# Kernel tuning notes

Measured on AMD Instinct MI355X. Metric: run time of the kernel, lower is better.

The kernel has to match this reference:

```python
import jax, jax.numpy as jnp
from jax import lax
import numpy as np
import math

B, LBL, PRED, CIN = 16, 48, 336, 7
L = LBL + PRED
DM, E = 512, 2
DIN, N, DCONV = 2 * DM, 16, 4
DTR = math.ceil(DM / 16)  # 32
TF = 4  # freq='h' time features
EPS = 1e-5


def _ln(x, w, b):
    m = x.mean(-1, keepdims=True)
    v = ((x - m) ** 2).mean(-1, keepdims=True)
    return (x - m) / jnp.sqrt(v + EPS) * w + b


def _silu(x):
    return x * jax.nn.sigmoid(x)


def _token_embed(x, w):
    # Conv1d(c_in, d_model, k=3, padding=1, circular, bias=False). x: (B,L,C), w: (DM,C,3)
    xp = jnp.concatenate([x[:, -1:], x, x[:, :1]], axis=1)  # circular pad along L
    y = lax.conv_general_dilated(xp.transpose(0, 2, 1), w, (1,), 'VALID',
                                 dimension_numbers=('NCH', 'OIH', 'NCH'))
    return y.transpose(0, 2, 1)  # (B,L,DM)


def _selective_scan(u, dt, A, Bm, Cm):
    # u,dt: (B,L,DIN); A: (DIN,N); Bm,Cm: (B,L,N)
    h0 = jnp.zeros((u.shape[0], DIN, N), u.dtype)

    def step(h, inp):
        u_t, dt_t, B_t, C_t = inp  # (B,DIN),(B,DIN),(B,N),(B,N)
        dA = jnp.exp(dt_t[:, :, None] * A)  # (B,DIN,N)
        h = dA * h + (dt_t * u_t)[:, :, None] * B_t[:, None, :]
        y = jnp.einsum('bdn,bn->bd', h, C_t)
        return h, y

    _, ys = lax.scan(step, h0, (u.transpose(1, 0, 2), dt.transpose(1, 0, 2),
                                Bm.transpose(1, 0, 2), Cm.transpose(1, 0, 2)))
    return ys.transpose(1, 0, 2)  # (B,L,DIN)


def _mamba(x, p):
    (in_w, conv_w, conv_b, xproj_w, dtproj_w, dtproj_b, A_log, Dp, out_w) = p
    xz = x @ in_w.T                      # (B,L,2*DIN)
    xin, z = jnp.split(xz, 2, axis=-1)
    # depthwise causal conv1d, kernel DCONV
    xt = jnp.pad(xin.transpose(0, 2, 1), ((0, 0), (0, 0), (DCONV - 1, 0)))
    xc = lax.conv_general_dilated(xt, conv_w, (1,), 'VALID', feature_group_count=DIN,
                                  dimension_numbers=('NCH', 'OIH', 'NCH'))
    xc = _silu((xc + conv_b[None, :, None]).transpose(0, 2, 1))  # (B,L,DIN)
    dbc = xc @ xproj_w.T                 # (B,L,DTR+2N)
    dt_r, Bm, Cm = dbc[..., :DTR], dbc[..., DTR:DTR + N], dbc[..., DTR + N:]
    dt = jax.nn.softplus(dt_r @ dtproj_w.T + dtproj_b)  # (B,L,DIN)
    A = -jnp.exp(A_log)                  # (DIN,N)
    y = _selective_scan(xc, dt, A, Bm, Cm) + xc * Dp
    y = y * _silu(z)
    return y @ out_w.T                   # (B,L,DM)


def _model(x_dec, x_mark_dec, token_w, timef_w, layer_ps, fin_w, fin_b, out_w):
    mean = lax.stop_gradient(x_dec[:, :LBL].mean(1, keepdims=True))
    head = x_dec[:, :LBL] - mean
    std = lax.stop_gradient(jnp.sqrt(head.var(axis=1, keepdims=True) + EPS))
    head = head / std
    xd = jnp.concatenate([head, x_dec[:, LBL:]], axis=1)
    x = _token_embed(xd, token_w) + x_mark_dec @ timef_w.T  # DataEmbedding_wo_pos (eval: no dropout)
    for i in range(E):
        nw, nb = layer_ps[0][i], layer_ps[1][i]
        mp = tuple(layer_ps[j][i] for j in range(2, 11))
        x = x + _mamba(_ln(x, nw, nb), mp)
    x = _ln(x, fin_w, fin_b)
    out = x @ out_w.T
    out = out * std + mean
    return out[:, -PRED:, :]


def setup_inputs() -> dict:
    key = jax.random.key(0)
    ks = jax.random.split(key, 20)
    s = 0.02
    d = {
        'x_enc': jax.random.normal(ks[0], (B, 96, CIN), jnp.float32),
        'x_mark_enc': jax.random.normal(ks[1], (B, 96, TF), jnp.float32),
        'x_dec': jax.random.normal(ks[2], (B, L, CIN), jnp.float32),
        'x_mark_dec': jax.random.normal(ks[3], (B, L, TF), jnp.float32),
        'token_w': jax.random.normal(ks[4], (DM, CIN, 3), jnp.float32) * s,
        'timef_w': jax.random.normal(ks[5], (DM, TF), jnp.float32) * s,
        'norm_w': jnp.ones((E, DM), jnp.float32),
        'norm_b': jnp.zeros((E, DM), jnp.float32),
        'in_proj_w': jax.random.normal(ks[6], (E, 2 * DIN, DM), jnp.float32) * s,
        'conv_w': jax.random.normal(ks[7], (E, DIN, 1, DCONV), jnp.float32) * s,
        'conv_b': jnp.zeros((E, DIN), jnp.float32),
        'xproj_w': jax.random.normal(ks[8], (E, DTR + 2 * N, DIN), jnp.float32) * s,
        'dtproj_w': jax.random.normal(ks[9], (E, DIN, DTR), jnp.float32) * s,
        'dtproj_b': jnp.full((E, DIN), -4.0, jnp.float32),
        'A_log': jnp.tile(jnp.log(jnp.arange(1, N + 1, dtype=jnp.float32)), (E, DIN, 1)),
        'D': jnp.ones((E, DIN), jnp.float32),
        'outproj_w': jax.random.normal(ks[10], (E, DM, DIN), jnp.float32) * s,
        'final_norm_w': jnp.ones((DM,), jnp.float32),
        'final_norm_b': jnp.zeros((DM,), jnp.float32),
        'out_w': jax.random.normal(ks[11], (CIN, DM), jnp.float32) * s,
    }
    return d


def reference(x_enc, x_mark_enc, x_dec, x_mark_dec, token_w, timef_w, norm_w, norm_b,
              in_proj_w, conv_w, conv_b, xproj_w, dtproj_w, dtproj_b, A_log, D,
              outproj_w, final_norm_w, final_norm_b, out_w):
    layer_ps = (norm_w, norm_b, in_proj_w, conv_w, conv_b, xproj_w, dtproj_w,
                dtproj_b, A_log, D, outproj_w)
    return _model(x_dec, x_mark_dec, token_w, timef_w, layer_ps,
                  final_norm_w, final_norm_b, out_w)
```

## Files before the change

### kernel.cpp

```cpp
#include <hip/hip_runtime.h>

#define B_    16
#define LBL_  48
#define PRED_ 336
#define CIN_  7
#define L_    384
#define DM_   512
#define E_    2
#define DIN_  1024
#define N_    16
#define DCONV_ 4
#define DTR_  32
#define TF_   4
#define EPSF  1e-5f
#define NSEG  16
#define SEGL  24
#define SC2   2
#define NCHK  12

typedef unsigned short u16;
typedef __attribute__((ext_vector_type(8))) short short8;
typedef __attribute__((ext_vector_type(4))) float f32x4;

__device__ __forceinline__ float bf2f(u16 u){
  union { float f; unsigned int i; } cv; cv.i = ((unsigned int)u) << 16; return cv.f;
}
__device__ __forceinline__ u16 f2bf(float f){
  union { float f; unsigned int i; } cv; cv.f = f;
  unsigned int x = cv.i;
  unsigned int lsb = (x >> 16) & 1u;
  x += 0x7fffu + lsb;
  return (u16)(x >> 16);
}
__device__ __forceinline__ float lo16(unsigned int v){
  union { float f; unsigned int i; } cv; cv.i = v << 16; return cv.f;
}
__device__ __forceinline__ float hi16(unsigned int v){
  union { float f; unsigned int i; } cv; cv.i = v & 0xffff0000u; return cv.f;
}

#define GLDS(g, l) __builtin_amdgcn_global_load_lds( \
    (const __attribute__((address_space(1))) void*)(g), \
    (__attribute__((address_space(3))) void*)(l), 16, 0, 0)

#define PO_XDEC   0
#define PO_XMARK  43008
#define PO_TOKW   67584
#define PO_TIMEF  78336
#define PO_NORMW  80384
#define PO_NORMB  81408
#define PO_INW    82432
#define PO_CONVW  2179584
#define PO_CONVB  2187776
#define PO_XPROJ  2189824
#define PO_DTW    2320896
#define PO_DTB    2386432
#define PO_ALOG   2388480
#define PO_DP     2421248
#define PO_OUTW   2423296
#define PO_FNW    3471872
#define PO_FNB    3472384
#define PO_HEADW  3472896
#define P_TOTAL   3476480
#define A_X    3476480
#define A_LNB  6622208
#define A_XZ   9767936
#define A_DT   22350848
#define A_DBCS 28642304
#define A_MEAN 29078528
#define A_STD  29078640
#define A_XCB_OFF 3145728

struct Ptrs { const void* p[18]; };

__device__ __forceinline__ float wredsum(float s){
  #pragma unroll
  for (int off = 32; off; off >>= 1) s += __shfl_xor(s, off, 64);
  return s;
}

__device__ __forceinline__ void qpowers(float q, float* p){
  float q2 = q*q;
  float q4 = q2*q2;
  float q8 = q4*q4;
  float q3 = q2*q;
  p[0]=q;      p[1]=q2;     p[2]=q3;     p[3]=q4;
  p[4]=q4*q;   p[5]=q4*q2;  p[6]=q4*q3;  p[7]=q8;
  p[8]=q8*q;   p[9]=q8*q2;  p[10]=q8*q3; p[11]=q8*q4;
  p[12]=q8*p[4]; p[13]=q8*p[5]; p[14]=q8*p[6]; p[15]=q8*q8;
}

__device__ __forceinline__ unsigned int xcd_swz(unsigned int bid, unsigned int nwg){
  return (bid & 7u) * (nwg >> 3) + (bid >> 3);
}

__global__ __launch_bounds__(256) void convert_kernel(Ptrs ps, float* __restrict__ dst){
  const int offs[18] = {PO_XDEC, PO_XMARK, PO_TOKW, PO_TIMEF, PO_NORMW, PO_NORMB,
                        PO_INW, PO_CONVW, PO_CONVB, PO_XPROJ, PO_DTW, PO_DTB,
                        PO_ALOG, PO_DP, PO_OUTW, PO_FNW, PO_FNB, PO_HEADW};
  int idx = blockIdx.x * 256 + threadIdx.x;
  if (idx >= P_TOTAL) return;
  int seg = 0;
  #pragma unroll
  for (int s = 1; s < 18; s++) if (idx >= offs[s]) seg = s;
  int off = idx - offs[seg];
  int isbf = (((const u16*)ps.p[4])[0] == 0x3F80u);
  if (seg == 6 || seg == 9 || seg == 10 || seg == 14){
    u16 hv = isbf ? ((const u16*)ps.p[seg])[off]
                  : f2bf(((const float*)ps.p[seg])[off]);
    ((u16*)(dst + offs[seg]))[off] = hv;
  } else {
    float v = isbf ? bf2f(((const u16*)ps.p[seg])[off])
                   : ((const float*)ps.p[seg])[off];
    dst[idx] = v;
  }
}

__global__ __launch_bounds__(256) void embed_ln_kernel(const float* __restrict__ x_dec,
      const float* __restrict__ token_w, const float* __restrict__ x_mark,
      const float* __restrict__ timef_w, const float* __restrict__ nw,
      const float* __restrict__ nb, float* __restrict__ x, u16* __restrict__ out,
      float* __restrict__ meanv, float* __restrict__ stdv){
  __shared__ float sm[8], siv[8], ssd[8];
  int wv = threadIdx.x >> 6;
  int lane = threadIdx.x & 63;
  int tok = blockIdx.x*4 + wv;
  int t = tok % L_;
  int b = tok / L_;
  for (int c = wv; c < CIN_; c += 4){
    float v0 = (lane < LBL_) ? x_dec[(b*L_+lane)*CIN_+c] : 0.f;
    float m = wredsum(v0) * (1.f/LBL_);
    float dv = (lane < LBL_) ? (v0 - m) : 0.f;
    float sd = sqrtf(wredsum(dv*dv) * (1.f/LBL_) + EPSF);
    if (lane == 0){ sm[c] = m; siv[c] = 1.f/sd; ssd[c] = sd; }
  }
  __syncthreads();
  if ((blockIdx.x % (L_/4)) == 0 && threadIdx.x < CIN_){
    meanv[b*CIN_ + threadIdx.x] = sm[threadIdx.x];
    stdv[b*CIN_ + threadIdx.x]  = ssd[threadIdx.x];
  }
  int tm1 = (t == 0) ? L_-1 : t-1;
  int tp1 = (t == L_-1) ? 0 : t+1;
  auto ldx = [&](int row, int c){
    float v = x_dec[(b*L_+row)*CIN_+c];
    return (row < LBL_) ? (v - sm[c]) * siv[c] : v;
  };
  const float* mk = x_mark + (b*L_+t)*TF_;
  float a0[CIN_], a1[CIN_], a2[CIN_], mkv[TF_];
  #pragma unroll
  for (int ci = 0; ci < CIN_; ci++){ a0[ci]=ldx(tm1,ci); a1[ci]=ldx(t,ci); a2[ci]=ldx(tp1,ci); }
  #pragma unroll
  for (int f = 0; f < TF_; f++) mkv[f] = mk[f];
  float v[8];
  #pragma unroll
  for (int j = 0; j < 8; j++){
    int d = lane*8 + j;
    float acc = 0.f;
    #pragma unroll
    for (int ci = 0; ci < CIN_; ci++){
      const float* w = token_w + (d*CIN_+ci)*3;
      acc += a0[ci]*w[0] + a1[ci]*w[1] + a2[ci]*w[2];
    }
    #pragma unroll
    for (int f = 0; f < TF_; f++)
      acc += mkv[f] * timef_w[d*TF_+f];
    v[j] = acc;
  }
  float* xr = x + (size_t)tok*DM_ + lane*8;
  *(float4*)xr       = (float4){v[0],v[1],v[2],v[3]};
  *(float4*)(xr + 4) = (float4){v[4],v[5],v[6],v[7]};
  float s = (v[0]+v[1])+(v[2]+v[3])+((v[4]+v[5])+(v[6]+v[7]));
  float mean = wredsum(s) * (1.f/DM_);
  float s2 = 0.f;
  #pragma unroll
  for (int j = 0; j < 8; j++){ v[j] -= mean; s2 += v[j]*v[j]; }
  float rstd = rsqrtf(wredsum(s2) * (1.f/DM_) + EPSF);
  const float* wr = nw + lane*8;
  const float* br = nb + lane*8;
  uint4 o; unsigned int* op = (unsigned int*)&o;
  #pragma unroll
  for (int k = 0; k < 4; k++){
    u16 e0 = f2bf(v[2*k]   * rstd * wr[2*k]   + br[2*k]);
    u16 e1 = f2bf(v[2*k+1] * rstd * wr[2*k+1] + br[2*k+1]);
    op[k] = (unsigned int)e0 | ((unsigned int)e1 << 16);
  }
  *(uint4*)(out + (size_t)tok*DM_ + lane*8) = o;
}

__global__ __launch_bounds__(256) void ln_kernel(const float* __restrict__ x,
     const float* __restrict__ w, const float* __restrict__ bias, u16* __restrict__ out){
  int tok = blockIdx.x*4 + (threadIdx.x >> 6);
  int lane = threadIdx.x & 63;
  const float* xr = x + (size_t)tok*DM_ + lane*8;
  float4 a = *(const float4*)xr;
  float4 bq = *(const float4*)(xr + 4);
  float v[8] = {a.x,a.y,a.z,a.w,bq.x,bq.y,bq.z,bq.w};
  float s = (v[0]+v[1])+(v[2]+v[3])+((v[4]+v[5])+(v[6]+v[7]));
  float mean = wredsum(s) * (1.f/DM_);
  float s2 = 0.f;
  #pragma unroll
  for (int j = 0; j < 8; j++){ v[j] -= mean; s2 += v[j]*v[j]; }
  float rstd = rsqrtf(wredsum(s2) * (1.f/DM_) + EPSF);
  const float* wr = w + lane*8;
  const float* br = bias + lane*8;
  uint4 o; unsigned int* op = (unsigned int*)&o;
  #pragma unroll
  for (int k = 0; k < 4; k++){
    u16 e0 = f2bf(v[2*k]   * rstd * wr[2*k]   + br[2*k]);
    u16 e1 = f2bf(v[2*k+1] * rstd * wr[2*k+1] + br[2*k+1]);
    op[k] = (unsigned int)e0 | ((unsigned int)e1 << 16);
  }
  *(uint4*)(out + (size_t)tok*DM_ + lane*8) = o;
}

__global__ __launch_bounds__(256) void inproj_conv(const u16* __restrict__ A,
    const u16* __restrict__ Wt, const float* __restrict__ cw, const float* __restrict__ cb,
    u16* __restrict__ xz, u16* __restrict__ xcb){
  __shared__ u16 As[384 * 64];
  __shared__ u16 Ws[64 * 64];
  int tid = threadIdx.x;
  int wv = tid >> 6, lane = tid & 63;
  unsigned int bid = blockIdx.y * 32 + blockIdx.x;
  unsigned int swz = xcd_swz(bid, 512);
  int b  = (int)(swz >> 5);
  int n0 = (int)(swz & 31) * 64;
  int m0 = b * L_;
  int la = lane & 15, lk = lane >> 4;
  f32x4 acc[6][4];
  #pragma unroll
  for (int i = 0; i < 6; i++)
    #pragma unroll
    for (int j = 0; j < 4; j++) acc[i][j] = (f32x4){0.f,0.f,0.f,0.f};
  int sr = lane >> 3;
  int sc = (((lane & 7) ^ (sr & 7)) * 8);
  const u16* Ag = A + (size_t)(m0 + wv*96 + sr) * DM_ + sc;
  u16* Al = As + (wv*96)*64 + lane*8;
  const u16* Wg = Wt + (size_t)(n0 + wv*16 + sr) * DM_ + sc;
  u16* Wl = Ws + (wv*16)*64 + lane*8;
  for (int k0 = 0; k0 < DM_; k0 += 64){
    #pragma unroll
    for (int i = 0; i < 12; i++) GLDS(Ag + (size_t)(i*8)*DM_ + k0, Al + i*512);
    #pragma unroll
    for (int i = 0; i < 2; i++)  GLDS(Wg + (size_t)(i*8)*DM_ + k0, Wl + i*512);
    __syncthreads();
    #pragma unroll
    for (int ks = 0; ks < 2; ks++){
      int ch = (ks*4 + lk) ^ (la & 7);
      short8 af[6], bfr[4];
      #pragma unroll
      for (int mi = 0; mi < 6; mi++) af[mi] = *(const short8*)&As[(wv*96 + mi*16 + la)*64 + ch*8];
      #pragma unroll
      for (int ni = 0; ni < 4; ni++) bfr[ni] = *(const short8*)&Ws[(ni*16 + la)*64 + ch*8];
      #pragma unroll
      for (int mi = 0; mi < 6; mi++)
        #pragma unroll
        for (int ni = 0; ni < 4; ni++)
          acc[mi][ni] = __builtin_amdgcn_mfma_f32_16x16x32_bf16(af[mi], bfr[ni], acc[mi][ni], 0, 0, 0);
    }
    __syncthreads();
  }
  #pragma unroll
  for (int mi = 0; mi < 6; mi++)
    #pragma unroll
    for (int ni = 0; ni < 4; ni++){
      int colc = ni*2 + (la >> 3);
      #pragma unroll
      for (int r = 0; r < 4; r++){
        int row = wv*96 + mi*16 + lk*4 + r;
        As[row*64 + ((colc ^ (row & 7))<<3) + (la & 7)] = f2bf(acc[mi][ni][r]);
      }
    }
  __syncthreads();
  int c8 = (tid & 7) * 8;
  int tg = tid >> 3;
  if (n0 < DIN_){
    float4 w[8]; float bias[8];
    #pragma unroll
    for (int k = 0; k < 8; k++){
      w[k] = *(const float4*)(cw + (n0 + c8 + k)*4);
      bias[k] = cb[n0 + c8 + k];
    }
    for (int i = 0; i < 12; i++){
      int t = tg*12 + i;
      uint4 tap[4];
      #pragma unroll
      for (int j = 0; j < 4; j++){
        int rr = t - 3 + j;
        if (rr >= 0)
          tap[j] = *(const uint4*)&As[rr*64 + ((((c8>>3) ^ (rr & 7)))<<3)];
      }
      float v[8];
      #pragma unroll
      for (int k = 0; k < 8; k++){
        float s = bias[k];
        #pragma unroll
        for (int j = 0; j < 4; j++){
          if (j >= 3 - t){
            const unsigned int* tp = (const unsigned int*)&tap[j];
            float xv = (k & 1) ? hi16(tp[k >> 1]) : lo16(tp[k >> 1]);
            s += xv * ((const float*)&w[k])[j];
          }
        }
        v[k] = s / (1.f + __expf(-s));
      }
      uint4 o; unsigned int* op = (unsigned int*)&o;
      #pragma unroll
      for (int k = 0; k < 4; k++)
        op[k] = (unsigned int)f2bf(v[2*k]) | ((unsigned int)f2bf(v[2*k+1]) << 16);
      *(uint4*)(xcb + (size_t)(m0 + t)*DIN_ + n0 + c8) = o;
    }
  } else {
    for (int i = 0; i < 12; i++){
      int t = tg*12 + i;
      uint4 vq = *(const uint4*)&As[t*64 + ((((c8>>3) ^ (t & 7)))<<3)];
      *(uint4*)(xz + (size_t)(m0 + t)*(2*DIN_) + n0 + c8) = vq;
    }
  }
}

template<int TN, int ACCUM, int BF16OUT>
__global__ __launch_bounds__(256) void gemm_mfma(const u16* __restrict__ A, const u16* __restrict__ Wt,
    void* __restrict__ C, int M, int N, int K){
  constexpr int WN = TN / 2;
  constexpr int NI = WN / 16;
  __shared__ u16 As[128 * 64];
  __shared__ u16 Ws[TN * 64];
  int tid = threadIdx.x;
  int wv = tid >> 6, lane = tid & 63;
  int wm = (wv & 1) * 64, wn = (wv >> 1) * WN;
  unsigned int gx = gridDim.x;
  unsigned int bid = blockIdx.y * gx + blockIdx.x;
  unsigned int swz = xcd_swz(bid, gx * gridDim.y);
  int m0 = (int)(swz / gx) * 128, n0 = (int)(swz % gx) * TN;
  int la = lane & 15, lk = lane >> 4;
  f32x4 acc[4][NI];
  #pragma unroll
  for (int i = 0; i < 4; i++)
    #pragma unroll
    for (int j = 0; j < NI; j++) acc[i][j] = (f32x4){0.f, 0.f, 0.f, 0.f};
  int sr = lane >> 3;
  int sc = (((lane & 7) ^ (sr & 7)) * 8);
  const u16* Ag = A + (size_t)(m0 + wv*32 + sr) * K + sc;
  u16* Al = As + (wv*32)*64 + lane*8;
  const u16 *Wg; u16 *Wl;
  if constexpr (TN == 128){
    Wg = Wt + (size_t)(n0 + wv*32 + sr) * K + sc;
    Wl = Ws + (wv*32)*64 + lane*8;
  } else {
    Wg = Wt + (size_t)(n0 + wv*16 + sr) * K + sc;
    Wl = Ws + (wv*16)*64 + lane*8;
  }
  for (int k0 = 0; k0 < K; k0 += 64){
    #pragma unroll
    for (int i = 0; i < 4; i++) GLDS(Ag + (size_t)(i*8)*K + k0, Al + i*512);
    if constexpr (TN == 128){
      #pragma unroll
      for (int i = 0; i < 4; i++) GLDS(Wg + (size_t)(i*8)*K + k0, Wl + i*512);
    } else {
      #pragma unroll
      for (int i = 0; i < 2; i++) GLDS(Wg + (size_t)(i*8)*K + k0, Wl + i*512);
    }
    __syncthreads();
    #pragma unroll
    for (int ks = 0; ks < 2; ks++){
      short8 af[4], bfr[NI];
      int ch = (ks*4 + lk) ^ (la & 7);
      #pragma unroll
      for (int mi = 0; mi < 4; mi++) af[mi] = *(const short8*)&As[(wm + mi*16 + la)*64 + ch*8];
      #pragma unroll
      for (int ni = 0; ni < NI; ni++) bfr[ni] = *(const short8*)&Ws[(wn + ni*16 + la)*64 + ch*8];
      #pragma unroll
      for (int mi = 0; mi < 4; mi++)
        #pragma unroll
        for (int ni = 0; ni < NI; ni++)
          acc[mi][ni] = __builtin_amdgcn_mfma_f32_16x16x32_bf16(af[mi], bfr[ni], acc[mi][ni], 0, 0, 0);
    }
    __syncthreads();
  }
  #pragma unroll
  for (int mi = 0; mi < 4; mi++)
    #pragma unroll
    for (int ni = 0; ni < NI; ni++){
      int row = m0 + wm + mi*16 + lk*4;
      int col = n0 + wn + ni*16 + la;
      #pragma unroll
      for (int r = 0; r < 4; r++){
        if constexpr (BF16OUT){
          u16* p = (u16*)C + (size_t)row * N + col;
          p[(size_t)r * N] = f2bf(acc[mi][ni][r]);
        } else {
          float* p = (float*)C + (size_t)row * N + col;
          if (ACCUM) p[(size_t)r * N] += acc[mi][ni][r];
          else       p[(size_t)r * N]  = acc[mi][ni][r];
        }
      }
    }
}

__global__ __launch_bounds__(256) void xdt_mfma(const u16* __restrict__ A,
    const u16* __restrict__ Wt, const u16* __restrict__ dtwb, const float* __restrict__ dtb,
    u16* __restrict__ dt, float* __restrict__ dbcs){
  __shared__ u16 As[32 * 64];
  __shared__ u16 Ws[64 * 64];
  __shared__ float Ds[32 * 66];
  __shared__ u16 Wd[64 * 32];
  __shared__ u16 Db[32 * 72];
  int tid = threadIdx.x;
  int wv = tid >> 6, lane = tid & 63;
  unsigned int swz = xcd_swz(blockIdx.x, 192);
  int m0 = (int)swz * 32;
  int la = lane & 15, lk = lane >> 4;
  int wm = (wv & 1) * 16, wn = (wv >> 1) * 32;

  f32x4 acc[2];
  acc[0] = (f32x4){0.f,0.f,0.f,0.f};
  acc[1] = (f32x4){0.f,0.f,0.f,0.f};
  int sr = lane >> 3;
  int sc = (((lane & 7) ^ (sr & 7)) * 8);
  const u16* Ag = A + (size_t)(m0 + wv*8 + sr) * DIN_ + sc;
  u16* Al = As + (wv*8)*64 + lane*8;
  const u16* Wg0 = Wt + (size_t)(wv*16 + sr) * DIN_ + sc;
  const u16* Wg1 = Wt + (size_t)(wv*16 + 8 + sr) * DIN_ + sc;
  u16* Wl0 = Ws + (wv*16)*64 + lane*8;
  u16* Wl1 = Ws + (wv*16 + 8)*64 + lane*8;
  for (int k0 = 0; k0 < DIN_; k0 += 64){
    GLDS(Ag + k0, Al);
    GLDS(Wg0 + k0, Wl0);
    GLDS(Wg1 + k0, Wl1);
    __syncthreads();
    #pragma unroll
    for (int ks = 0; ks < 2; ks++){
      int ch = (ks*4 + lk) ^ (la & 7);
      short8 af = *(const short8*)&As[(wm + la)*64 + ch*8];
      #pragma unroll
      for (int ni = 0; ni < 2; ni++){
        short8 bfr = *(const short8*)&Ws[(wn + ni*16 + la)*64 + ch*8];
        acc[ni] = __builtin_amdgcn_mfma_f32_16x16x32_bf16(af, bfr, acc[ni], 0, 0, 0);
      }
    }
    __syncthreads();
  }
  #pragma unroll
  for (int ni = 0; ni < 2; ni++)
    #pragma unroll
    for (int r = 0; r < 4; r++)
      Ds[(wm + lk*4 + r)*66 + wn + ni*16 + la] = acc[ni][r];
  __syncthreads();
  {
    int row = tid >> 3;
    int c4  = (tid & 7) * 4;
    float4 v = {Ds[row*66 + 32 + c4], Ds[row*66 + 33 + c4],
                Ds[row*66 + 34 + c4], Ds[row*66 + 35 + c4]};
    *(float4*)&dbcs[(size_t)(m0 + row)*32 + c4] = v;
  }
  short8 af2;
  {
    u16 tmp[8];
    #pragma unroll
    for (int i = 0; i < 8; i++)
      tmp[i] = f2bf(Ds[(wm + la)*66 + lk*8 + i]);
    af2 = *(const short8*)tmp;
  }

  int srd = lane >> 2;
  int scd = (((lane & 3) ^ (srd & 3)) * 8);
  for (int nt = 0; nt < 16; nt++){
    GLDS(dtwb + (size_t)(nt*64 + wv*16 + srd)*32 + scd, Wd + (wv*16)*32 + lane*8);
    __syncthreads();
    #pragma unroll
    for (int ni = 0; ni < 2; ni++){
      int rw = wn + ni*16 + la;
      int ch2 = (lk ^ (la & 3)) * 8;
      short8 bfr2 = *(const short8*)&Wd[rw*32 + ch2];
      f32x4 a2 = (f32x4){0.f,0.f,0.f,0.f};
      a2 = __builtin_amdgcn_mfma_f32_16x16x32_bf16(af2, bfr2, a2, 0, 0, 0);
      int d = nt*64 + wn + ni*16 + la;
      float bias = dtb[d];
      #pragma unroll
      for (int r = 0; r < 4; r++){
        float raw = a2[r] + bias;
        float sp = (raw > 20.f) ? raw : __logf(1.f + __expf(raw));
        Db[(wm + lk*4 + r)*72 + wn + ni*16 + la] = f2bf(sp);
      }
    }
    __syncthreads();
    int row = tid >> 3;
    int c8  = (tid & 7) * 8;
    uint4 o = *(const uint4*)&Db[row*72 + c8];
    *(uint4*)&dt[(size_t)(m0 + row)*DIN_ + nt*64 + c8] = o;
  }
}

#define WSTR2 896
__global__ __launch_bounds__(1024, 1) void scan_kernel(
    u16* __restrict__ ub_yb,
    const float* __restrict__ dbcs, const u16* __restrict__ xz,
    const u16* __restrict__ dtp,
    const float* __restrict__ A_log, const float* __restrict__ Dp){
  __shared__ float smem[16384];

  int tid = threadIdx.x;
  int lane = tid & 63;
  int seg  = tid >> 6;
  int b = blockIdx.x >> 4;
  int g = blockIdx.x & 15;
  int d = g*64 + lane;
  size_t base = (size_t)b * L_;

  float* wbase = smem + seg * WSTR2;
  float* sbc = wbase;
  float* su  = wbase + 128;
  float* sz  = wbase + 384;
  float* sdt = wbase + 640;

  int st = lane >> 5;
  int j  = lane & 31;

  float A[16];
  #pragma unroll
  for (int n = 0; n < 16; n += 4){
    float4 av = *(const float4*)(A_log + (size_t)d*N_ + n);
    A[n] = -__expf(av.x); A[n+1] = -__expf(av.y); A[n+2] = -__expf(av.z); A[n+3] = -__expf(av.w);
  }
  float Dv = Dp[d];
  bool fastA = true;
  #pragma unroll
  for (int n = 0; n < 16; n++) fastA = fastA && (fabsf(A[n] + (float)(n+1)) < 1e-3f*(n+1));

  float h[16];
  #pragma unroll
  for (int n = 0; n < 16; n++) h[n] = 0.f;

  auto ldc = [&](int c, float& kbc, unsigned int& ku, unsigned int& kz,
                 unsigned int& kt, bool wz){
    size_t tokr = base + seg*SEGL + c*SC2 + st;
    kbc = dbcs[tokr*32 + j];
    ku  = ((const unsigned int*)(ub_yb + tokr*DIN_ + g*64))[j];
    kt  = ((const unsigned int*)(dtp + tokr*DIN_ + g*64))[j];
    if (wz) kz = ((const unsigned int*)(xz + tokr*(2*DIN_) + DIN_ + g*64))[j];
  };
  auto stc = [&](int buf, float kbc, unsigned int ku, unsigned int kz,
                 unsigned int kt, bool wz){
    sbc[buf*64 + st*32 + j] = kbc;
    su [buf*128 + st*64 + 2*j]     = lo16(ku);
    su [buf*128 + st*64 + 2*j + 1] = hi16(ku);
    sdt[buf*128 + st*64 + 2*j]     = lo16(kt);
    sdt[buf*128 + st*64 + 2*j + 1] = hi16(kt);
    if (wz){
      sz[buf*128 + st*64 + 2*j]     = lo16(kz);
      sz[buf*128 + st*64 + 2*j + 1] = hi16(kz);
    }
  };

  float S = 0.f;
  {
    float kbc; unsigned int ku, kz, kt;
    ldc(0, kbc, ku, kz, kt, false);
    stc(0, kbc, ku, kz, kt, false);
    for (int c = 0; c < NCHK; c++){
      int cur = c & 1;
      bool have = (c + 1 < NCHK);
      float nbc; unsigned int nu, nz, nt;
      if (have) ldc(c+1, nbc, nu, nz, nt, false);
      for (int s = 0; s < SC2; s++){
        float dtv = sdt[cur*128 + s*64 + lane];
        float u   = su [cur*128 + s*64 + lane];
        const float* bcrow = sbc + cur*64 + s*32;
        float Bf[16];
        #pragma unroll
        for (int i = 0; i < 16; i += 4){
          float4 bv = *(const float4*)(bcrow + i);
          Bf[i] = bv.x; Bf[i+1] = bv.y; Bf[i+2] = bv.z; Bf[i+3] = bv.w;
        }
        float du = dtv * u;
        S += dtv;
        if (fastA){
          float q = __expf(-dtv);
          float p[16];
          qpowers(q, p);
          #pragma unroll
          for (int n = 0; n < 16; n++) h[n] = p[n] * h[n] + du * Bf[n];
        } else {
          #pragma unroll
          for (int n = 0; n < 16; n++){
            float dA = __expf(dtv * A[n]);
            h[n] = dA * h[n] + du * Bf[n];
          }
        }
      }
      if (have) stc(1 - cur, nbc, nu, nz, nt, false);
    }
  }

  #pragma unroll
  for (int half = 0; half < 2; half++){
    __syncthreads();
    #pragma unroll
    for (int n = 0; n < 8; n++){
      int nn = half*8 + n;
      smem[(n*NSEG + seg)*64 + lane]        = h[nn];
      smem[8192 + (n*NSEG + seg)*64 + lane] = __expf(A[nn] * S);
    }
    __syncthreads();
    float hs[8];
    #pragma unroll
    for (int n = 0; n < 8; n++) hs[n] = 0.f;
    for (int jj = 0; jj < seg; jj++){
      #pragma unroll
      for (int n = 0; n < 8; n++){
        float qh = smem[(n*NSEG + jj)*64 + lane];
        float qP = smem[8192 + (n*NSEG + jj)*64 + lane];
        hs[n] = qh + qP * hs[n];
      }
    }
    #pragma unroll
    for (int n = 0; n < 8; n++) h[half*8 + n] = hs[n];
  }
  __syncthreads();

  {
    float kbc; unsigned int ku, kz, kt;
    ldc(0, kbc, ku, kz, kt, true);
    stc(0, kbc, ku, kz, kt, true);
    for (int c = 0; c < NCHK; c++){
      int cur = c & 1;
      bool have = (c + 1 < NCHK);
      float nbc; unsigned int nu, nz, nt;
      if (have) ldc(c+1, nbc, nu, nz, nt, true);
      for (int s = 0; s < SC2; s++){
        float dtv = sdt[cur*128 + s*64 + lane];
        float u   = su [cur*128 + s*64 + lane];
        float z   = sz [cur*128 + s*64 + lane];
        const float* bcrow = sbc + cur*64 + s*32;
        float Bf[16], Cf[16];
        #pragma unroll
        for (int i = 0; i < 16; i += 4){
          float4 bv = *(const float4*)(bcrow + i);
          float4 cv = *(const float4*)(bcrow + 16 + i);
          Bf[i] = bv.x; Bf[i+1] = bv.y; Bf[i+2] = bv.z; Bf[i+3] = bv.w;
          Cf[i] = cv.x; Cf[i+1] = cv.y; Cf[i+2] = cv.z; Cf[i+3] = cv.w;
        }
        float du = dtv * u;
        float acc = 0.f;
        if (fastA){
          float q = __expf(-dtv);
          float p[16];
          qpowers(q, p);
          #pragma unroll
          for (int n = 0; n < 16; n++){
            h[n] = p[n] * h[n] + du * Bf[n];
            acc += h[n] * Cf[n];
          }
        } else {
          #pragma unroll
          for (int n = 0; n < 16; n++){
            float dA = __expf(dtv * A[n]);
            h[n] = dA * h[n] + du * Bf[n];
            acc += h[n] * Cf[n];
          }
        }
        float y = acc + u * Dv;
        size_t tok = base + seg*SEGL + c*SC2 + s;
        ub_yb[tok*DIN_ + d] = f2bf(y * (z / (1.f + __expf(-z))));
      }
      if (have) stc(1 - cur, nbc, nu, nz, nt, true);
    }
  }
}

__global__ __launch_bounds__(256) void head_kernel(const float* __restrict__ x,
    const float* __restrict__ fw, const float* __restrict__ fb, const float* __restrict__ ow,
    const float* __restrict__ meanv, const float* __restrict__ stdv, void* __restrict__ out,
    const u16* __restrict__ dtype_probe){
  int wav = blockIdx.x*4 + (threadIdx.x >> 6);
  int lane = threadIdx.x & 63;
  if (wav >= B_*PRED_) return;
  int b = wav / PRED_;
  int tt = wav % PRED_;
  int tok = b*L_ + LBL_ + tt;
  const float* xr = x + (size_t)tok*DM_ + lane*8;
  float4 a = *(const float4*)xr;
  float4 bq = *(const float4*)(xr + 4);
  float v[8] = {a.x,a.y,a.z,a.w,bq.x,bq.y,bq.z,bq.w};
  float s = (v[0]+v[1])+(v[2]+v[3])+((v[4]+v[5])+(v[6]+v[7]));
  float mean = wredsum(s) * (1.f/DM_);
  float s2 = 0.f;
  #pragma unroll
  for (int j = 0; j < 8; j++){ v[j] -= mean; s2 += v[j]*v[j]; }
  float rstd = rsqrtf(wredsum(s2) * (1.f/DM_) + EPSF);
  const float* fwr = fw + lane*8;
  const float* fbr = fb + lane*8;
  #pragma unroll
  for (int j = 0; j < 8; j++) v[j] = v[j] * rstd * fwr[j] + fbr[j];
  int isbf = (dtype_probe[0] == 0x3F80u);
  for (int o = 0; o < CIN_; o++){
    const float* owr = ow + (size_t)o*DM_ + lane*8;
    float part = 0.f;
    #pragma unroll
    for (int j = 0; j < 8; j++) part += v[j] * owr[j];
    part = wredsum(part);
    if (lane == 0){
      float res = part * stdv[b*CIN_ + o] + meanv[b*CIN_ + o];
      size_t oidx = (size_t)(b*PRED_ + tt)*CIN_ + o;
      if (isbf) ((u16*)out)[oidx] = f2bf(res);
      else      ((float*)out)[oidx] = res;
    }
  }
}

extern "C" void kernel_launch(void* const* d_in, const int* in_sizes, int n_in,
                              void* d_out, int out_size, void* d_ws, size_t ws_size,
                              hipStream_t stream){
  float* P = (float*)d_ws;

  Ptrs ps;
  for (int i = 0; i < 18; i++) ps.p[i] = d_in[2 + i];

  float* x    = P + A_X;
  u16*   lnxb = (u16*)(P + A_LNB);
  u16*   xz   = (u16*)(P + A_XZ);
  u16*   dt   = (u16*)(P + A_DT);
  u16*   xcb  = (u16*)(P + A_DT + A_XCB_OFF);
  float* dbcs = P + A_DBCS;
  float* meanv= P + A_MEAN;
  float* stdv = P + A_STD;
  const u16* bwi = (const u16*)(P + PO_INW);
  const u16* bwx = (const u16*)(P + PO_XPROJ);
  const u16* bwd = (const u16*)(P + PO_DTW);
  const u16* bwo = (const u16*)(P + PO_OUTW);

  convert_kernel<<<(P_TOTAL+255)/256, 256, 0, stream>>>(ps, P);
  embed_ln_kernel<<<(B_*L_)/4, 256, 0, stream>>>(
      P + PO_XDEC, P + PO_TOKW, P + PO_XMARK, P + PO_TIMEF,
      P + PO_NORMW, P + PO_NORMB, x, lnxb, meanv, stdv);

  for (int e = 0; e < E_; e++){
    if (e > 0)
      ln_kernel<<<(B_*L_)/4, 256, 0, stream>>>(x, P + PO_NORMW + e*DM_, P + PO_NORMB + e*DM_, lnxb);
    inproj_conv<<<dim3(32, 16), 256, 0, stream>>>(
        lnxb, bwi + (size_t)e*2*DIN_*DM_,
        P + PO_CONVW + e*DIN_*DCONV_, P + PO_CONVB + e*DIN_, xz, xcb);
    xdt_mfma<<<192, 256, 0, stream>>>(
        xcb, bwx + (size_t)e*64*DIN_, bwd + (size_t)e*DIN_*DTR_,
        P + PO_DTB + e*DIN_, dt, dbcs);
    scan_kernel<<<256, 1024, 0, stream>>>(
        xcb, dbcs, xz, dt, P + PO_ALOG + e*DIN_*N_, P + PO_DP + e*DIN_);
    gemm_mfma<64,1,0><<<dim3(DM_/64, (B_*L_)/128), 256, 0, stream>>>(
        xcb, bwo + (size_t)e*DM_*DIN_, x, B_*L_, DM_, DIN_);
  }

  head_kernel<<<(B_*PRED_+3)/4, 256, 0, stream>>>(
      x, P + PO_FNW, P + PO_FNB, P + PO_HEADW, meanv, stdv, d_out, (const u16*)d_in[6]);
}
```

Before: 379.5 us.

## Fuse parameter conversion into embedding kernel, vectorize conversion, reuse conv taps

Merges the weight-conversion kernel and the embedding/LayerNorm kernel into one launch. Embedding blocks read raw inputs directly in either dtype, and the remaining blocks convert parameters 8 elements per thread with vector loads and stores. The depthwise conv now slides a register window of taps instead of reloading four rows from LDS for each timestep. The head kernel batches its seven warp reductions into one interleaved shuffle loop. The cost is extra dtype branching inside the embedding path, and the conversion code now assumes every segment is aligned to 8 elements.

```diff
diff --git a/kernel.cpp b/kernel.cpp
--- a/kernel.cpp
+++ b/kernel.cpp
@@ -71,12 +71,21 @@
 #define A_STD  29078640
 #define A_XCB_OFF 3145728
 
+#define EMB_NB  ((B_*L_)/4)
+#define CV_BASE PO_NORMW
+#define CV_ELEMS (P_TOTAL - CV_BASE)
+#define CV_NB   ((CV_ELEMS + 2047)/2048)
+
 struct Ptrs { const void* p[18]; };
 
 __device__ __forceinline__ float wredsum(float s){
   #pragma unroll
   for (int off = 32; off; off >>= 1) s += __shfl_xor(s, off, 64);
   return s;
+}
+
+__device__ __forceinline__ float ldraw(const void* p, int i, int isbf){
+  return isbf ? bf2f(((const u16*)p)[i]) : ((const float*)p)[i];
 }
 
 __device__ __forceinline__ void qpowers(float q, float* p){
@@ -94,33 +103,58 @@
   return (bid & 7u) * (nwg >> 3) + (bid >> 3);
 }
 
-__global__ __launch_bounds__(256) void convert_kernel(Ptrs ps, float* __restrict__ dst){
-  const int offs[18] = {PO_XDEC, PO_XMARK, PO_TOKW, PO_TIMEF, PO_NORMW, PO_NORMB,
-                        PO_INW, PO_CONVW, PO_CONVB, PO_XPROJ, PO_DTW, PO_DTB,
-                        PO_ALOG, PO_DP, PO_OUTW, PO_FNW, PO_FNB, PO_HEADW};
-  int idx = blockIdx.x * 256 + threadIdx.x;
-  if (idx >= P_TOTAL) return;
-  int seg = 0;
-  #pragma unroll
-  for (int s = 1; s < 18; s++) if (idx >= offs[s]) seg = s;
-  int off = idx - offs[seg];
+__global__ __launch_bounds__(256) void prep_embed_convert(Ptrs ps, float* __restrict__ dst,
+      float* __restrict__ x, u16* __restrict__ out,
+      float* __restrict__ meanv, float* __restrict__ stdv){
   int isbf = (((const u16*)ps.p[4])[0] == 0x3F80u);
-  if (seg == 6 || seg == 9 || seg == 10 || seg == 14){
-    u16 hv = isbf ? ((const u16*)ps.p[seg])[off]
-                  : f2bf(((const float*)ps.p[seg])[off]);
-    ((u16*)(dst + offs[seg]))[off] = hv;
-  } else {
-    float v = isbf ? bf2f(((const u16*)ps.p[seg])[off])
-                   : ((const float*)ps.p[seg])[off];
-    dst[idx] = v;
-  }
-}
-
-__global__ __launch_bounds__(256) void embed_ln_kernel(const float* __restrict__ x_dec,
-      const float* __restrict__ token_w, const float* __restrict__ x_mark,
-      const float* __restrict__ timef_w, const float* __restrict__ nw,
-      const float* __restrict__ nb, float* __restrict__ x, u16* __restrict__ out,
-      float* __restrict__ meanv, float* __restrict__ stdv){
+  if ((int)blockIdx.x >= EMB_NB){
+    int idx0 = CV_BASE + ((int)blockIdx.x - EMB_NB)*2048 + (int)threadIdx.x*8;
+    if (idx0 >= P_TOTAL) return;
+    const int offs[14] = {PO_NORMW, PO_NORMB, PO_INW, PO_CONVW, PO_CONVB, PO_XPROJ,
+                          PO_DTW, PO_DTB, PO_ALOG, PO_DP, PO_OUTW, PO_FNW, PO_FNB, PO_HEADW};
+    const int wseg[14] = {0,0,1,0,0,1,1,0,0,0,1,0,0,0};
+    int seg = 0;
+    #pragma unroll
+    for (int s = 1; s < 14; s++) if (idx0 >= offs[s]) seg = s;
+    int off = idx0 - offs[seg];
+    const void* src = ps.p[seg + 4];
+    if (wseg[seg]){
+      if (isbf){
+        uint4 v = *(const uint4*)((const u16*)src + off);
+        *(uint4*)((u16*)(dst + offs[seg]) + off) = v;
+      } else {
+        float4 f0 = *(const float4*)((const float*)src + off);
+        float4 f1 = *(const float4*)((const float*)src + off + 4);
+        uint4 o; unsigned int* op = (unsigned int*)&o;
+        op[0] = (unsigned int)f2bf(f0.x) | ((unsigned int)f2bf(f0.y) << 16);
+        op[1] = (unsigned int)f2bf(f0.z) | ((unsigned int)f2bf(f0.w) << 16);
+        op[2] = (unsigned int)f2bf(f1.x) | ((unsigned int)f2bf(f1.y) << 16);
+        op[3] = (unsigned int)f2bf(f1.z) | ((unsigned int)f2bf(f1.w) << 16);
+        *(uint4*)((u16*)(dst + offs[seg]) + off) = o;
+      }
+    } else {
+      if (isbf){
+        uint4 v = *(const uint4*)((const u16*)src + off);
+        const u16* pv = (const u16*)&v;
+        float4 o0 = {bf2f(pv[0]), bf2f(pv[1]), bf2f(pv[2]), bf2f(pv[3])};
+        float4 o1 = {bf2f(pv[4]), bf2f(pv[5]), bf2f(pv[6]), bf2f(pv[7])};
+        *(float4*)(dst + idx0)     = o0;
+        *(float4*)(dst + idx0 + 4) = o1;
+      } else {
+        float4 f0 = *(const float4*)((const float*)src + off);
+        float4 f1 = *(const float4*)((const float*)src + off + 4);
+        *(float4*)(dst + idx0)     = f0;
+        *(float4*)(dst + idx0 + 4) = f1;
+      }
+    }
+    return;
+  }
+  const void* x_dec  = ps.p[0];
+  const void* x_mark = ps.p[1];
+  const void* tokw   = ps.p[2];
+  const void* timef  = ps.p[3];
+  const void* nw     = ps.p[4];
+  const void* nb     = ps.p[5];
   __shared__ float sm[8], siv[8], ssd[8];
   int wv = threadIdx.x >> 6;
   int lane = threadIdx.x & 63;
@@ -128,7 +162,7 @@
   int t = tok % L_;
   int b = tok / L_;
   for (int c = wv; c < CIN_; c += 4){
-    float v0 = (lane < LBL_) ? x_dec[(b*L_+lane)*CIN_+c] : 0.f;
+    float v0 = (lane < LBL_) ? ldraw(x_dec, (b*L_+lane)*CIN_+c, isbf) : 0.f;
     float m = wredsum(v0) * (1.f/LBL_);
     float dv = (lane < LBL_) ? (v0 - m) : 0.f;
     float sd = sqrtf(wredsum(dv*dv) * (1.f/LBL_) + EPSF);
@@ -142,15 +176,14 @@
   int tm1 = (t == 0) ? L_-1 : t-1;
   int tp1 = (t == L_-1) ? 0 : t+1;
   auto ldx = [&](int row, int c){
-    float v = x_dec[(b*L_+row)*CIN_+c];
+    float v = ldraw(x_dec, (b*L_+row)*CIN_+c, isbf);
     return (row < LBL_) ? (v - sm[c]) * siv[c] : v;
   };
-  const float* mk = x_mark + (b*L_+t)*TF_;
   float a0[CIN_], a1[CIN_], a2[CIN_], mkv[TF_];
   #pragma unroll
   for (int ci = 0; ci < CIN_; ci++){ a0[ci]=ldx(tm1,ci); a1[ci]=ldx(t,ci); a2[ci]=ldx(tp1,ci); }
   #pragma unroll
-  for (int f = 0; f < TF_; f++) mkv[f] = mk[f];
+  for (int f = 0; f < TF_; f++) mkv[f] = ldraw(x_mark, (b*L_+t)*TF_+f, isbf);
   float v[8];
   #pragma unroll
   for (int j = 0; j < 8; j++){
@@ -158,12 +191,13 @@
     float acc = 0.f;
     #pragma unroll
     for (int ci = 0; ci < CIN_; ci++){
-      const float* w = token_w + (d*CIN_+ci)*3;
-      acc += a0[ci]*w[0] + a1[ci]*w[1] + a2[ci]*w[2];
+      int wb = (d*CIN_+ci)*3;
+      acc += a0[ci]*ldraw(tokw, wb, isbf) + a1[ci]*ldraw(tokw, wb+1, isbf)
+           + a2[ci]*ldraw(tokw, wb+2, isbf);
     }
     #pragma unroll
     for (int f = 0; f < TF_; f++)
-      acc += mkv[f] * timef_w[d*TF_+f];
+      acc += mkv[f] * ldraw(timef, d*TF_+f, isbf);
     v[j] = acc;
   }
   float* xr = x + (size_t)tok*DM_ + lane*8;
@@ -175,13 +209,12 @@
   #pragma unroll
   for (int j = 0; j < 8; j++){ v[j] -= mean; s2 += v[j]*v[j]; }
   float rstd = rsqrtf(wredsum(s2) * (1.f/DM_) + EPSF);
-  const float* wr = nw + lane*8;
-  const float* br = nb + lane*8;
   uint4 o; unsigned int* op = (unsigned int*)&o;
   #pragma unroll
   for (int k = 0; k < 4; k++){
-    u16 e0 = f2bf(v[2*k]   * rstd * wr[2*k]   + br[2*k]);
-    u16 e1 = f2bf(v[2*k+1] * rstd * wr[2*k+1] + br[2*k+1]);
+    int d0 = lane*8 + 2*k;
+    u16 e0 = f2bf(v[2*k]   * rstd * ldraw(nw, d0,   isbf) + ldraw(nb, d0,   isbf));
+    u16 e1 = f2bf(v[2*k+1] * rstd * ldraw(nw, d0+1, isbf) + ldraw(nb, d0+1, isbf));
     op[k] = (unsigned int)e0 | ((unsigned int)e1 << 16);
   }
   *(uint4*)(out + (size_t)tok*DM_ + lane*8) = o;
@@ -280,14 +313,21 @@
       w[k] = *(const float4*)(cw + (n0 + c8 + k)*4);
       bias[k] = cb[n0 + c8 + k];
     }
+    uint4 tap[4];
+    {
+      int t0 = tg*12;
+      #pragma unroll
+      for (int j = 0; j < 4; j++){
+        int rr = t0 - 3 + j;
+        if (rr >= 0)
+          tap[j] = *(const uint4*)&As[rr*64 + ((((c8>>3) ^ (rr & 7)))<<3)];
+      }
+    }
     for (int i = 0; i < 12; i++){
       int t = tg*12 + i;
-      uint4 tap[4];
-      #pragma unroll
-      for (int j = 0; j < 4; j++){
-        int rr = t - 3 + j;
-        if (rr >= 0)
-          tap[j] = *(const uint4*)&As[rr*64 + ((((c8>>3) ^ (rr & 7)))<<3)];
+      if (i > 0){
+        tap[0] = tap[1]; tap[1] = tap[2]; tap[2] = tap[3];
+        tap[3] = *(const uint4*)&As[t*64 + ((((c8>>3) ^ (t & 7)))<<3)];
       }
       float v[8];
       #pragma unroll
@@ -693,14 +733,23 @@
   #pragma unroll
   for (int j = 0; j < 8; j++) v[j] = v[j] * rstd * fwr[j] + fbr[j];
   int isbf = (dtype_probe[0] == 0x3F80u);
+  float part[CIN_];
+  #pragma unroll
   for (int o = 0; o < CIN_; o++){
     const float* owr = ow + (size_t)o*DM_ + lane*8;
-    float part = 0.f;
-    #pragma unroll
-    for (int j = 0; j < 8; j++) part += v[j] * owr[j];
-    part = wredsum(part);
-    if (lane == 0){
-      float res = part * stdv[b*CIN_ + o] + meanv[b*CIN_ + o];
+    float p = 0.f;
+    #pragma unroll
+    for (int j = 0; j < 8; j++) p += v[j] * owr[j];
+    part[o] = p;
+  }
+  #pragma unroll
+  for (int off = 32; off; off >>= 1)
+    #pragma unroll
+    for (int o = 0; o < CIN_; o++) part[o] += __shfl_xor(part[o], off, 64);
+  if (lane == 0){
+    #pragma unroll
+    for (int o = 0; o < CIN_; o++){
+      float res = part[o] * stdv[b*CIN_ + o] + meanv[b*CIN_ + o];
       size_t oidx = (size_t)(b*PRED_ + tt)*CIN_ + o;
       if (isbf) ((u16*)out)[oidx] = f2bf(res);
       else      ((float*)out)[oidx] = res;
@@ -729,10 +778,8 @@
   const u16* bwd = (const u16*)(P + PO_DTW);
   const u16* bwo = (const u16*)(P + PO_OUTW);
 
-  convert_kernel<<<(P_TOTAL+255)/256, 256, 0, stream>>>(ps, P);
-  embed_ln_kernel<<<(B_*L_)/4, 256, 0, stream>>>(
-      P + PO_XDEC, P + PO_TOKW, P + PO_XMARK, P + PO_TIMEF,
-      P + PO_NORMW, P + PO_NORMB, x, lnxb, meanv, stdv);
+  prep_embed_convert<<<EMB_NB + CV_NB, 256, 0, stream>>>(
+      ps, P, x, lnxb, meanv, stdv);
 
   for (int e = 0; e < E_; e++){
     if (e > 0)
```

Result: slower. 488.2 us (+28.6%).

## Vectorize weight conversion, slide conv taps in registers, batch head reductions

Applied to the files above, without the earlier changes.

The convert kernel now has each thread handle 8 elements with 128-bit loads and stores, and the grid shrinks to match. This assumes every segment offset and length is a multiple of 8, otherwise the tail of a segment may be copied from the wrong source. The depthwise conv in inproj_conv now keeps a sliding window of taps in registers and loads one new row from LDS per step instead of four. The head kernel reduces all seven output channels in one interleaved shuffle tree instead of seven serial wave reductions.

```diff
diff --git a/kernel.cpp b/kernel.cpp
--- a/kernel.cpp
+++ b/kernel.cpp
@@ -95,24 +95,48 @@
 }
 
 __global__ __launch_bounds__(256) void convert_kernel(Ptrs ps, float* __restrict__ dst){
+  int idx = (blockIdx.x * 256 + threadIdx.x) * 8;
+  if (idx >= P_TOTAL) return;
   const int offs[18] = {PO_XDEC, PO_XMARK, PO_TOKW, PO_TIMEF, PO_NORMW, PO_NORMB,
                         PO_INW, PO_CONVW, PO_CONVB, PO_XPROJ, PO_DTW, PO_DTB,
                         PO_ALOG, PO_DP, PO_OUTW, PO_FNW, PO_FNB, PO_HEADW};
-  int idx = blockIdx.x * 256 + threadIdx.x;
-  if (idx >= P_TOTAL) return;
-  int seg = 0;
-  #pragma unroll
-  for (int s = 1; s < 18; s++) if (idx >= offs[s]) seg = s;
-  int off = idx - offs[seg];
+  const int w16t[18] = {0,0,0,0,0,0,1,0,0,1,1,0,0,0,1,0,0,0};
   int isbf = (((const u16*)ps.p[4])[0] == 0x3F80u);
-  if (seg == 6 || seg == 9 || seg == 10 || seg == 14){
-    u16 hv = isbf ? ((const u16*)ps.p[seg])[off]
-                  : f2bf(((const float*)ps.p[seg])[off]);
-    ((u16*)(dst + offs[seg]))[off] = hv;
+  int base = 0, w16 = 0;
+  const void* src = ps.p[0];
+  #pragma unroll
+  for (int s = 1; s < 18; s++){
+    if (idx >= offs[s]){ base = offs[s]; src = ps.p[s]; w16 = w16t[s]; }
+  }
+  int off = idx - base;
+  if (w16){
+    if (isbf){
+      uint4 v = *(const uint4*)((const u16*)src + off);
+      *(uint4*)((u16*)(dst + base) + off) = v;
+    } else {
+      float4 f0 = *(const float4*)((const float*)src + off);
+      float4 f1 = *(const float4*)((const float*)src + off + 4);
+      uint4 o; unsigned int* op = (unsigned int*)&o;
+      op[0] = (unsigned int)f2bf(f0.x) | ((unsigned int)f2bf(f0.y) << 16);
+      op[1] = (unsigned int)f2bf(f0.z) | ((unsigned int)f2bf(f0.w) << 16);
+      op[2] = (unsigned int)f2bf(f1.x) | ((unsigned int)f2bf(f1.y) << 16);
+      op[3] = (unsigned int)f2bf(f1.z) | ((unsigned int)f2bf(f1.w) << 16);
+      *(uint4*)((u16*)(dst + base) + off) = o;
+    }
   } else {
-    float v = isbf ? bf2f(((const u16*)ps.p[seg])[off])
-                   : ((const float*)ps.p[seg])[off];
-    dst[idx] = v;
+    if (isbf){
+      uint4 v = *(const uint4*)((const u16*)src + off);
+      const u16* pv = (const u16*)&v;
+      float4 o0 = {bf2f(pv[0]), bf2f(pv[1]), bf2f(pv[2]), bf2f(pv[3])};
+      float4 o1 = {bf2f(pv[4]), bf2f(pv[5]), bf2f(pv[6]), bf2f(pv[7])};
+      *(float4*)(dst + idx)     = o0;
+      *(float4*)(dst + idx + 4) = o1;
+    } else {
+      float4 f0 = *(const float4*)((const float*)src + off);
+      float4 f1 = *(const float4*)((const float*)src + off + 4);
+      *(float4*)(dst + idx)     = f0;
+      *(float4*)(dst + idx + 4) = f1;
+    }
   }
 }
 
@@ -280,14 +304,21 @@
       w[k] = *(const float4*)(cw + (n0 + c8 + k)*4);
       bias[k] = cb[n0 + c8 + k];
     }
+    uint4 tap[4];
+    {
+      int t0 = tg*12;
+      #pragma unroll
+      for (int j = 0; j < 4; j++){
+        int rr = t0 - 3 + j;
+        if (rr >= 0)
+          tap[j] = *(const uint4*)&As[rr*64 + ((((c8>>3) ^ (rr & 7)))<<3)];
+      }
+    }
     for (int i = 0; i < 12; i++){
       int t = tg*12 + i;
-      uint4 tap[4];
-      #pragma unroll
-      for (int j = 0; j < 4; j++){
-        int rr = t - 3 + j;
-        if (rr >= 0)
-          tap[j] = *(const uint4*)&As[rr*64 + ((((c8>>3) ^ (rr & 7)))<<3)];
+      if (i > 0){
+        tap[0] = tap[1]; tap[1] = tap[2]; tap[2] = tap[3];
+        tap[3] = *(const uint4*)&As[t*64 + ((((c8>>3) ^ (t & 7)))<<3)];
       }
       float v[8];
       #pragma unroll
@@ -693,14 +724,23 @@
   #pragma unroll
   for (int j = 0; j < 8; j++) v[j] = v[j] * rstd * fwr[j] + fbr[j];
   int isbf = (dtype_probe[0] == 0x3F80u);
+  float part[CIN_];
+  #pragma unroll
   for (int o = 0; o < CIN_; o++){
     const float* owr = ow + (size_t)o*DM_ + lane*8;
-    float part = 0.f;
-    #pragma unroll
-    for (int j = 0; j < 8; j++) part += v[j] * owr[j];
-    part = wredsum(part);
-    if (lane == 0){
-      float res = part * stdv[b*CIN_ + o] + meanv[b*CIN_ + o];
+    float p = 0.f;
+    #pragma unroll
+    for (int j = 0; j < 8; j++) p += v[j] * owr[j];
+    part[o] = p;
+  }
+  #pragma unroll
+  for (int off = 32; off; off >>= 1)
+    #pragma unroll
+    for (int o = 0; o < CIN_; o++) part[o] += __shfl_xor(part[o], off, 64);
+  if (lane == 0){
+    #pragma unroll
+    for (int o = 0; o < CIN_; o++){
+      float res = part[o] * stdv[b*CIN_ + o] + meanv[b*CIN_ + o];
       size_t oidx = (size_t)(b*PRED_ + tt)*CIN_ + o;
       if (isbf) ((u16*)out)[oidx] = f2bf(res);
       else      ((float*)out)[oidx] = res;
@@ -729,7 +769,7 @@
   const u16* bwd = (const u16*)(P + PO_DTW);
   const u16* bwo = (const u16*)(P + PO_OUTW);
 
-  convert_kernel<<<(P_TOTAL+255)/256, 256, 0, stream>>>(ps, P);
+  convert_kernel<<<(P_TOTAL/8 + 255)/256, 256, 0, stream>>>(ps, P);
   embed_ln_kernel<<<(B_*L_)/4, 256, 0, stream>>>(
       P + PO_XDEC, P + PO_TOKW, P + PO_XMARK, P + PO_TIMEF,
       P + PO_NORMW, P + PO_NORMB, x, lnxb, meanv, stdv);
```

After: 369.6 us (median of 2 runs). 1.03x faster.
